# Performance work log

Hardware: AMD Instinct MI355X
Metric: run time of the kernel (lower is better)

Reference implementation:

```python
import jax, jax.numpy as jnp
import numpy as np

_EPSILON = 1e-06

def _sparsemax(z):
    # sparsemax along last axis (Martins & Astudillo 2016, sort-based projection)
    m = z.shape[-1]
    z_sorted = jnp.flip(jnp.sort(z, axis=-1), axis=-1)          # descending
    z_cum = jnp.cumsum(z_sorted, axis=-1)
    r = jnp.arange(1, m + 1, dtype=z.dtype)
    support = (1.0 + r * z_sorted) > z_cum                       # [b, m]
    k = jnp.sum(support, axis=-1, keepdims=True)                 # support size, int
    tau = (jnp.take_along_axis(z_cum, k - 1, axis=-1) - 1.0) / k.astype(z.dtype)
    return jnp.maximum(z - tau, 0.0)

def setup_inputs() -> dict:
    key = jax.random.key(0)
    ks = jax.random.split(key, 4)
    b, m, d, out = 2048, 8192, 1024, 1000
    encoder_output = jax.random.normal(ks[0], (b, d), dtype=jnp.float32)
    memory_set = jax.random.normal(ks[1], (m, d), dtype=jnp.float32)
    W1 = jax.random.normal(ks[2], (d, 2 * d), dtype=jnp.float32) * (1.0 / np.sqrt(d))
    b1 = jnp.zeros((2 * d,), dtype=jnp.float32)
    W2 = jax.random.normal(ks[3], (2 * d, out), dtype=jnp.float32) * (1.0 / np.sqrt(2 * d))
    b2 = jnp.zeros((out,), dtype=jnp.float32)
    return {"encoder_output": encoder_output, "memory_set": memory_set,
            "W1": W1, "b1": b1, "W2": W2, "b2": b2}

def reference(encoder_output, memory_set, W1, b1, W2, b2):
    # cosine distance: 1 - x_hat @ y_hat^T  (with eps inside the sqrt, as in torch code)
    x_norm = encoder_output / jnp.sqrt(jnp.sum(encoder_output * encoder_output, axis=1, keepdims=True) + _EPSILON)
    y_norm = memory_set / jnp.sqrt(jnp.sum(memory_set * memory_set, axis=1, keepdims=True) + _EPSILON)
    dist = 1.0 - jnp.matmul(x_norm, y_norm.T)                    # [b, m]
    content_weights = _sparsemax(-dist)                          # [b, m]
    memory_vector = jnp.matmul(content_weights, memory_set)      # [b, d]
    h = jax.nn.relu(jnp.matmul(memory_vector, W1) + b1)          # [b, 2d]
    output = jnp.matmul(h, W2) + b2                              # [b, out]
    return output
```

## Files before the change

kernel.cpp:

```cpp
#include <hip/hip_runtime.h>
#include <hip/hip_bf16.h>


#define TPB 256
#define CAP 1024
#define BK 64

typedef __bf16 bf16x8 __attribute__((ext_vector_type(8)));
typedef float  f32x4  __attribute__((ext_vector_type(4)));

typedef const __attribute__((address_space(1))) void* gas_ptr;
typedef __attribute__((address_space(3))) void*       las_ptr;

__device__ __forceinline__ unsigned short f2bf(float f) {
    __hip_bfloat16 h = __float2bfloat16(f);
    union { __hip_bfloat16 h; unsigned short s; } u; u.h = h; return u.s;
}
__device__ __forceinline__ float bf2f(unsigned short s) {
    union { unsigned int b; float f; } u; u.b = (unsigned int)s << 16; return u.f;
}
__device__ __forceinline__ unsigned short f2h(float f) {
    union { _Float16 h; unsigned short s; } u; u.h = (_Float16)f; return u.s;
}
__device__ __forceinline__ float h2f(unsigned short s) {
    union { unsigned short s; _Float16 h; } u; u.s = s; return (float)u.h;
}

__device__ __forceinline__ float block_reduce_sum(float v, float* sred) {
    #pragma unroll
    for (int off = 32; off > 0; off >>= 1) v += __shfl_down(v, off, 64);
    int lane = threadIdx.x & 63, wid = threadIdx.x >> 6;
    if (lane == 0) sred[wid] = v;
    __syncthreads();
    if (threadIdx.x == 0) sred[0] = sred[0] + sred[1] + sred[2] + sred[3];
    __syncthreads();
    float r = sred[0];
    __syncthreads();
    return r;
}

__device__ __forceinline__ void block_reduce_sum2(float& a, float& b, float* sred) {
    #pragma unroll
    for (int off = 32; off > 0; off >>= 1) {
        a += __shfl_down(a, off, 64);
        b += __shfl_down(b, off, 64);
    }
    int lane = threadIdx.x & 63, wid = threadIdx.x >> 6;
    if (lane == 0) { sred[wid] = a; sred[4 + wid] = b; }
    __syncthreads();
    if (threadIdx.x == 0) {
        sred[0] = sred[0] + sred[1] + sred[2] + sred[3];
        sred[4] = sred[4] + sred[5] + sred[6] + sred[7];
    }
    __syncthreads();
    a = sred[0]; b = sred[4];
    __syncthreads();
}

__global__ __launch_bounds__(TPB) void normalize_rows_bf16(const float* __restrict__ X0,
                                                           unsigned short* __restrict__ Y0,
                                                           const float* __restrict__ X1,
                                                           unsigned short* __restrict__ Y1,
                                                           float* __restrict__ norms1,
                                                           int nrow0, int cols) {
    __shared__ float sred[4];
    int r = blockIdx.x, tid = threadIdx.x;
    const float* X; unsigned short* Y; float* nn; int row;
    if (r < nrow0) { X = X0; Y = Y0; nn = nullptr; row = r; }
    else           { X = X1; Y = Y1; nn = norms1; row = r - nrow0; }
    const float4* x4 = (const float4*)(X + (size_t)row * cols);
    ushort4* y4 = (ushort4*)(Y + (size_t)row * cols);
    int n4 = cols >> 2;
    float ss = 0.f;
    for (int i = tid; i < n4; i += TPB) {
        float4 v = x4[i];
        ss += v.x * v.x + v.y * v.y + v.z * v.z + v.w * v.w;
    }
    float tot = block_reduce_sum(ss, sred);
    float nrm = sqrtf(tot + 1e-6f);
    float inv = 1.0f / nrm;
    if (nn && tid == 0) nn[row] = nrm;
    for (int i = tid; i < n4; i += TPB) {
        float4 v = x4[i];
        ushort4 o;
        o.x = f2bf(v.x * inv); o.y = f2bf(v.y * inv);
        o.z = f2bf(v.z * inv); o.w = f2bf(v.w * inv);
        y4[i] = o;
    }
}

__global__ __launch_bounds__(TPB) void transpose_cast(const float* __restrict__ in,
                                                      unsigned short* __restrict__ out,
                                                      int R, int C, int Cpad) {
    __shared__ float t[32][33];
    int x = threadIdx.x & 31, y = threadIdx.x >> 5;
    int r0 = blockIdx.y * 32, c0 = blockIdx.x * 32;
    #pragma unroll
    for (int yy = y; yy < 32; yy += 8) {
        int c = c0 + x;
        t[yy][x] = (c < C) ? in[(size_t)(r0 + yy) * C + c] : 0.f;
    }
    __syncthreads();
    #pragma unroll
    for (int yy = y; yy < 32; yy += 8) {
        int c = c0 + yy;
        if (c < Cpad)
            out[(size_t)c * R + r0 + x] = f2bf(t[x][yy]);
    }
}

__global__ __launch_bounds__(TPB) void sparsemax_compact(unsigned short* __restrict__ Zh,
                                                         const float* __restrict__ ynorm,
                                                         int* __restrict__ cnt, int m) {
    __shared__ float sz[8192];
    __shared__ float sred[8];
    __shared__ unsigned short cidx[CAP];
    __shared__ float cval[CAP];
    __shared__ unsigned int lcnt, ocnt;
    int row = blockIdx.x, tid = threadIdx.x;
    unsigned short* zrow = Zh + (size_t)row * m;
    unsigned int* prow = (unsigned int*)zrow;
    const uint4* zr8 = (const uint4*)zrow;
    int n8 = m >> 3;

    float s = 0.f, q = 0.f;
    float4* sz4 = (float4*)sz;
    for (int i = tid; i < n8; i += TPB) {
        uint4 v = zr8[i];
        float4 a, bq;
        a.x = h2f((unsigned short)(v.x & 0xffffu)); a.y = h2f((unsigned short)(v.x >> 16));
        a.z = h2f((unsigned short)(v.y & 0xffffu)); a.w = h2f((unsigned short)(v.y >> 16));
        bq.x = h2f((unsigned short)(v.z & 0xffffu)); bq.y = h2f((unsigned short)(v.z >> 16));
        bq.z = h2f((unsigned short)(v.w & 0xffffu)); bq.w = h2f((unsigned short)(v.w >> 16));
        sz4[2 * i] = a; sz4[2 * i + 1] = bq;
        s += a.x + a.y + a.z + a.w + bq.x + bq.y + bq.z + bq.w;
        q += a.x * a.x + a.y * a.y + a.z * a.z + a.w * a.w
           + bq.x * bq.x + bq.y * bq.y + bq.z * bq.z + bq.w * bq.w;
    }
    if (tid == 0) { lcnt = 0; ocnt = 0; }
    block_reduce_sum2(s, q, sred);
    float fm   = (float)m;
    float mean = s / fm;
    float sig  = sqrtf(fmaxf(q / fm - mean * mean, 0.f));
    float tau_s = (s - 1.f) / fm;
    float tau_g = mean + 2.f * sig;

    float Sg = 0.f, cg = 0.f, Ss = 0.f, cs = 0.f;
    for (int i = tid; i < m; i += TPB) {
        float z = sz[i];
        if (z > tau_g) { Sg += z - tau_g; cg += 1.f; }
        if (z > tau_s) { Ss += z - tau_s; cs += 1.f; }
    }
    block_reduce_sum2(Sg, cg, sred);
    block_reduce_sum2(Ss, cs, sred);

    float tau_lb, S_act, c_act;
    if (Sg >= 1.f) { tau_lb = tau_g; S_act = Sg + cg * tau_g; c_act = cg; }
    else           { tau_lb = tau_s; S_act = Ss + cs * tau_s; c_act = cs; }
    float tau1 = (S_act - 1.f) / c_act;
    if (tau1 < tau_lb) tau1 = tau_lb;

    for (int i = tid; i < m; i += TPB) {
        float z = sz[i];
        if (z > tau1) {
            unsigned int slot = atomicAdd(&lcnt, 1u);
            if (slot < CAP) { cidx[slot] = (unsigned short)i; cval[slot] = z; }
        }
    }
    __syncthreads();

    if (lcnt <= CAP && lcnt > 0) {
        int n = (int)lcnt;
        float tau = tau1, prev = -1.f;
        for (int it = 0; it < 64; ++it) {
            float S = 0.f, c = 0.f;
            for (int j = tid; j < n; j += TPB) {
                float z = cval[j];
                if (z > tau) { S += z; c += 1.f; }
            }
            block_reduce_sum2(S, c, sred);
            if (c < 0.5f || c == prev) break;
            tau = (S - 1.f) / c; prev = c;
        }
        for (int j = tid; j < n; j += TPB) {
            float w = cval[j] - tau;
            if (w > 0.f) {
                int idx = (int)cidx[j];
                unsigned int slot = atomicAdd(&ocnt, 1u);
                prow[slot] = ((unsigned int)idx << 16) | (unsigned int)f2bf(w * ynorm[idx]);
            }
        }
        __syncthreads();
        if (tid == 0) cnt[row] = (int)ocnt;
    } else {
        float tau = tau1, prev = -1.f;
        for (int it = 0; it < 64; ++it) {
            float S = 0.f, c = 0.f;
            for (int i = tid; i < m; i += TPB) {
                float z = sz[i];
                if (z > tau) { S += z; c += 1.f; }
            }
            block_reduce_sum2(S, c, sred);
            if (c < 0.5f || c == prev) break;
            tau = (S - 1.f) / c; prev = c;
        }
        for (int i = tid; i < m; i += TPB) {
            float w = sz[i] - tau;
            if (w > 0.f) {
                unsigned int slot = atomicAdd(&ocnt, 1u);
                prow[slot] = ((unsigned int)i << 16) | (unsigned int)f2bf(w * ynorm[i]);
            }
        }
        __syncthreads();
        if (tid == 0) cnt[row] = (int)ocnt;
    }
}

__global__ __launch_bounds__(TPB) void sparse_mv(const unsigned int* __restrict__ packed,
                                                 const int* __restrict__ cnt,
                                                 const unsigned short* __restrict__ yn,
                                                 unsigned short* __restrict__ mv,
                                                 int pitchU, int d) {
    __shared__ unsigned int sl[TPB];
    int row = blockIdx.x, tid = threadIdx.x;
    const unsigned int* prow = packed + (size_t)row * pitchU;
    int n = cnt[row];
    int c0 = tid * 4;
    float acc0 = 0.f, acc1 = 0.f, acc2 = 0.f, acc3 = 0.f;
    for (int j0 = 0; j0 < n; j0 += TPB) {
        int chunk = min(TPB, n - j0);
        __syncthreads();
        if (tid < chunk) sl[tid] = prow[j0 + tid];
        __syncthreads();
        #pragma unroll 4
        for (int jj = 0; jj < chunk; ++jj) {
            unsigned int u = sl[jj];
            int idx = (int)(u >> 16);
            float w = bf2f((unsigned short)(u & 0xffffu));
            ushort4 v = *(const ushort4*)&yn[(size_t)idx * d + c0];
            acc0 += w * bf2f(v.x);
            acc1 += w * bf2f(v.y);
            acc2 += w * bf2f(v.z);
            acc3 += w * bf2f(v.w);
        }
    }
    ushort4 o;
    o.x = f2bf(acc0); o.y = f2bf(acc1); o.z = f2bf(acc2); o.w = f2bf(acc3);
    *(ushort4*)&mv[(size_t)row * d + c0] = o;
}

template <int BN, int OUTMODE, int RELU, int HASBIAS>
__global__ __launch_bounds__(TPB) void gemm_bt(const unsigned short* __restrict__ A,
                                               const unsigned short* __restrict__ B,
                                               const float* __restrict__ bias,
                                               void* __restrict__ C,
                                               int M, int K, int lda, int NOUT, int ldc) {
    constexpr int IT = (BN == 128) ? 4 : 2;
    __shared__ unsigned short lA[128 * BK];
    __shared__ unsigned short lB[BN * BK];
    int tid = threadIdx.x;
    int lane = tid & 63, wv = tid >> 6;
    int wm = (BN == 128) ? (wv & 1) * 64 : wv * 32;
    int wn = (BN == 128) ? (wv >> 1) * 64 : 0;
    int lr = lane & 15, kq = lane >> 4;

    int rowBase = blockIdx.y * 128;
    int colBase = blockIdx.x * BN;

    f32x4 acc[IT][4] = {};

    for (int k0 = 0; k0 < K; k0 += BK) {
        #pragma unroll
        for (int l = 0; l < 4; ++l) {
            int li = l * 256 + tid;
            int row = li >> 3, s0 = li & 7;
            int seg = s0 ^ (row & 7);
            const char* g = (const char*)(A + (size_t)(rowBase + row) * lda + k0) + seg * 16;
            __builtin_amdgcn_global_load_lds((gas_ptr)g, (las_ptr)((char*)lA + li * 16), 16, 0, 0);
        }
        #pragma unroll
        for (int l = 0; l < BN / 32; ++l) {
            int li = l * 256 + tid;
            int row = li >> 3, s0 = li & 7;
            int seg = s0 ^ (row & 7);
            const char* g = (const char*)(B + (size_t)(colBase + row) * K + k0) + seg * 16;
            __builtin_amdgcn_global_load_lds((gas_ptr)g, (las_ptr)((char*)lB + li * 16), 16, 0, 0);
        }
        __syncthreads();

        #pragma unroll
        for (int h = 0; h < 2; ++h) {
            bf16x8 av[IT], bv[4];
            #pragma unroll
            for (int i = 0; i < IT; ++i) {
                int row = wm + i * 16 + lr;
                av[i] = *(const bf16x8*)((const char*)lA + row * 128
                                         + ((((h << 2) | kq) ^ (row & 7)) * 16));
            }
            #pragma unroll
            for (int j = 0; j < 4; ++j) {
                int row = wn + j * 16 + lr;
                bv[j] = *(const bf16x8*)((const char*)lB + row * 128
                                         + ((((h << 2) | kq) ^ (row & 7)) * 16));
            }
            #pragma unroll
            for (int i = 0; i < IT; ++i)
                #pragma unroll
                for (int j = 0; j < 4; ++j)
                    acc[i][j] = __builtin_amdgcn_mfma_f32_16x16x32_bf16(av[i], bv[j], acc[i][j], 0, 0, 0);
        }
        __syncthreads();
    }

    float* Cf = (float*)C;
    unsigned short* Cb = (unsigned short*)C;
    #pragma unroll
    for (int j = 0; j < 4; ++j) {
        int col = colBase + wn + j * 16 + lr;
        if (col >= NOUT) continue;
        float bv_ = HASBIAS ? bias[col] : 0.f;
        #pragma unroll
        for (int i = 0; i < IT; ++i) {
            #pragma unroll
            for (int r = 0; r < 4; ++r) {
                int row = rowBase + wm + i * 16 + kq * 4 + r;
                float v = acc[i][j][r] + bv_;
                if (RELU) v = fmaxf(v, 0.f);
                if (OUTMODE == 0)      Cf[(size_t)row * ldc + col] = v;
                else if (OUTMODE == 1) Cb[(size_t)row * ldc + col] = f2bf(v);
                else                   Cb[(size_t)row * ldc + col] = f2h(v);
            }
        }
    }
}

extern "C" void kernel_launch(void* const* d_in, const int* in_sizes, int n_in,
                              void* d_out, int out_size, void* d_ws, size_t ws_size,
                              hipStream_t stream) {
    const float* enc = (const float*)d_in[0];
    const float* mem = (const float*)d_in[1];
    const float* W1  = (const float*)d_in[2];
    const float* b1  = (const float*)d_in[3];
    const float* W2  = (const float*)d_in[4];
    const float* b2  = (const float*)d_in[5];

    const int d    = in_sizes[3] / 2;
    const int b    = in_sizes[0] / d;
    const int m    = in_sizes[1] / d;
    const int d2   = in_sizes[3];
    const int outN = in_sizes[5];
    const int outPad = 1024;

    unsigned short* xn    = (unsigned short*)d_ws;
    unsigned short* yn    = xn  + (size_t)b * d;
    float*          ynorm = (float*)(yn + (size_t)m * d);
    unsigned short* W1T   = (unsigned short*)(ynorm + m);
    unsigned short* W2T   = W1T + (size_t)d2 * d;
    unsigned short* Zh    = W2T + (size_t)outPad * d2;
    int*            cnt   = (int*)(Zh + (size_t)b * m);
    unsigned short* mv    = (unsigned short*)(cnt + b);
    unsigned short* h     = mv + (size_t)b * d;

    normalize_rows_bf16<<<b + m, TPB, 0, stream>>>(enc, xn, mem, yn, ynorm, b, d);

    transpose_cast<<<dim3(d2 / 32, d / 32), TPB, 0, stream>>>(W1, W1T, d, d2, d2);
    transpose_cast<<<dim3(outPad / 32, d2 / 32), TPB, 0, stream>>>(W2, W2T, d2, outN, outPad);

    gemm_bt<128, 2, 0, 0><<<dim3(m / 128, b / 128), TPB, 0, stream>>>(xn, yn, nullptr, Zh,
                                                                      b, d, d, m, m);
    sparsemax_compact<<<b, TPB, 0, stream>>>(Zh, ynorm, cnt, m);

    sparse_mv<<<b, TPB, 0, stream>>>((const unsigned int*)Zh, cnt, yn, mv, m / 2, d);

    gemm_bt<64, 1, 1, 1><<<dim3(d2 / 64, b / 128), TPB, 0, stream>>>(mv, W1T, b1, h,
                                                                     b, d, d, d2, d2);
    gemm_bt<64, 0, 0, 1><<<dim3(outPad / 64, b / 128), TPB, 0, stream>>>(h, W2T, b2, d_out,
                                                                         b, d2, d2, outN, outN);
}
```

Before: 275.9 us.

## Fuse sparsemax with gather, retile GEMMs, merge transposes, vectorize epilogue stores

Merges the sparsemax and sparse matrix-vector kernels into one kernel that keeps z in LDS as fp16 and accumulates the weighted memory rows directly, removing the packed intermediate write and read. GEMMs are retemplated with BM/BN parameters, BK reduced to 32, larger 256x128 tiles with 512 threads for the distance GEMM, and shuffle-packed vector stores in the epilogue. The two weight transpose launches are merged into one. The changes trade a shorter K step (more syncs per tile) and different occupancy for fewer launches and less global traffic.

```diff
diff --git a/kernel.cpp b/kernel.cpp
--- a/kernel.cpp
+++ b/kernel.cpp
@@ -4,7 +4,6 @@
 
 #define TPB 256
 #define CAP 1024
-#define BK 64
 
 typedef __bf16 bf16x8 __attribute__((ext_vector_type(8)));
 typedef float  f32x4  __attribute__((ext_vector_type(4)));
@@ -89,12 +88,11 @@
     }
 }
 
-__global__ __launch_bounds__(TPB) void transpose_cast(const float* __restrict__ in,
-                                                      unsigned short* __restrict__ out,
-                                                      int R, int C, int Cpad) {
+__device__ __forceinline__ void tc_body(const float* in, unsigned short* out,
+                                        int R, int C, int Cpad, int bx, int by) {
     __shared__ float t[32][33];
     int x = threadIdx.x & 31, y = threadIdx.x >> 5;
-    int r0 = blockIdx.y * 32, c0 = blockIdx.x * 32;
+    int r0 = by * 32, c0 = bx * 32;
     #pragma unroll
     for (int yy = y; yy < 32; yy += 8) {
         int c = c0 + x;
@@ -109,35 +107,52 @@
     }
 }
 
-__global__ __launch_bounds__(TPB) void sparsemax_compact(unsigned short* __restrict__ Zh,
-                                                         const float* __restrict__ ynorm,
-                                                         int* __restrict__ cnt, int m) {
-    __shared__ float sz[8192];
+__global__ __launch_bounds__(TPB) void transpose_cast2(const float* __restrict__ in1,
+                                                       unsigned short* __restrict__ out1,
+                                                       int R1, int C1, int Cp1,
+                                                       const float* __restrict__ in2,
+                                                       unsigned short* __restrict__ out2,
+                                                       int R2, int C2, int Cp2,
+                                                       int nblk1) {
+    int bid = blockIdx.x;
+    if (bid < nblk1) {
+        int nx = Cp1 / 32;
+        tc_body(in1, out1, R1, C1, Cp1, bid % nx, bid / nx);
+    } else {
+        bid -= nblk1;
+        int nx = Cp2 / 32;
+        tc_body(in2, out2, R2, C2, Cp2, bid % nx, bid / nx);
+    }
+}
+
+__global__ __launch_bounds__(TPB) void sparsemax_gather(const unsigned short* __restrict__ Zh,
+                                                        const float* __restrict__ ynorm,
+                                                        const unsigned short* __restrict__ yn,
+                                                        unsigned short* __restrict__ mv,
+                                                        int m, int d) {
+    __shared__ unsigned short szh[8192];
     __shared__ float sred[8];
     __shared__ unsigned short cidx[CAP];
     __shared__ float cval[CAP];
-    __shared__ unsigned int lcnt, ocnt;
+    __shared__ unsigned int lcnt;
     int row = blockIdx.x, tid = threadIdx.x;
-    unsigned short* zrow = Zh + (size_t)row * m;
-    unsigned int* prow = (unsigned int*)zrow;
-    const uint4* zr8 = (const uint4*)zrow;
+    const uint4* zr8 = (const uint4*)(Zh + (size_t)row * m);
+    uint4* sz8 = (uint4*)szh;
     int n8 = m >> 3;
 
     float s = 0.f, q = 0.f;
-    float4* sz4 = (float4*)sz;
     for (int i = tid; i < n8; i += TPB) {
         uint4 v = zr8[i];
-        float4 a, bq;
-        a.x = h2f((unsigned short)(v.x & 0xffffu)); a.y = h2f((unsigned short)(v.x >> 16));
-        a.z = h2f((unsigned short)(v.y & 0xffffu)); a.w = h2f((unsigned short)(v.y >> 16));
-        bq.x = h2f((unsigned short)(v.z & 0xffffu)); bq.y = h2f((unsigned short)(v.z >> 16));
-        bq.z = h2f((unsigned short)(v.w & 0xffffu)); bq.w = h2f((unsigned short)(v.w >> 16));
-        sz4[2 * i] = a; sz4[2 * i + 1] = bq;
-        s += a.x + a.y + a.z + a.w + bq.x + bq.y + bq.z + bq.w;
-        q += a.x * a.x + a.y * a.y + a.z * a.z + a.w * a.w
-           + bq.x * bq.x + bq.y * bq.y + bq.z * bq.z + bq.w * bq.w;
-    }
-    if (tid == 0) { lcnt = 0; ocnt = 0; }
+        sz8[i] = v;
+        unsigned int ww[4] = {v.x, v.y, v.z, v.w};
+        #pragma unroll
+        for (int k = 0; k < 4; ++k) {
+            float a = h2f((unsigned short)(ww[k] & 0xffffu));
+            float bq = h2f((unsigned short)(ww[k] >> 16));
+            s += a + bq; q += a * a + bq * bq;
+        }
+    }
+    if (tid == 0) lcnt = 0;
     block_reduce_sum2(s, q, sred);
     float fm   = (float)m;
     float mean = s / fm;
@@ -146,10 +161,18 @@
     float tau_g = mean + 2.f * sig;
 
     float Sg = 0.f, cg = 0.f, Ss = 0.f, cs = 0.f;
-    for (int i = tid; i < m; i += TPB) {
-        float z = sz[i];
-        if (z > tau_g) { Sg += z - tau_g; cg += 1.f; }
-        if (z > tau_s) { Ss += z - tau_s; cs += 1.f; }
+    for (int i = tid; i < n8; i += TPB) {
+        uint4 v = sz8[i];
+        unsigned int ww[4] = {v.x, v.y, v.z, v.w};
+        #pragma unroll
+        for (int k = 0; k < 4; ++k) {
+            float a = h2f((unsigned short)(ww[k] & 0xffffu));
+            float bq = h2f((unsigned short)(ww[k] >> 16));
+            if (a > tau_g) { Sg += a - tau_g; cg += 1.f; }
+            if (a > tau_s) { Ss += a - tau_s; cs += 1.f; }
+            if (bq > tau_g) { Sg += bq - tau_g; cg += 1.f; }
+            if (bq > tau_s) { Ss += bq - tau_s; cs += 1.f; }
+        }
     }
     block_reduce_sum2(Sg, cg, sred);
     block_reduce_sum2(Ss, cs, sred);
@@ -161,7 +184,7 @@
     if (tau1 < tau_lb) tau1 = tau_lb;
 
     for (int i = tid; i < m; i += TPB) {
-        float z = sz[i];
+        float z = h2f(szh[i]);
         if (z > tau1) {
             unsigned int slot = atomicAdd(&lcnt, 1u);
             if (slot < CAP) { cidx[slot] = (unsigned short)i; cval[slot] = z; }
@@ -169,9 +192,11 @@
     }
     __syncthreads();
 
-    if (lcnt <= CAP && lcnt > 0) {
-        int n = (int)lcnt;
-        float tau = tau1, prev = -1.f;
+    int fast = (lcnt <= CAP && lcnt > 0);
+    float tau = tau1;
+    int n = (int)lcnt;
+    if (fast) {
+        float prev = -1.f;
         for (int it = 0; it < 64; ++it) {
             float S = 0.f, c = 0.f;
             for (int j = tid; j < n; j += TPB) {
@@ -184,151 +209,166 @@
         }
         for (int j = tid; j < n; j += TPB) {
             float w = cval[j] - tau;
-            if (w > 0.f) {
-                int idx = (int)cidx[j];
-                unsigned int slot = atomicAdd(&ocnt, 1u);
-                prow[slot] = ((unsigned int)idx << 16) | (unsigned int)f2bf(w * ynorm[idx]);
-            }
+            cval[j] = (w > 0.f) ? w * ynorm[cidx[j]] : 0.f;
         }
         __syncthreads();
-        if (tid == 0) cnt[row] = (int)ocnt;
     } else {
-        float tau = tau1, prev = -1.f;
+        float prev = -1.f;
         for (int it = 0; it < 64; ++it) {
             float S = 0.f, c = 0.f;
             for (int i = tid; i < m; i += TPB) {
-                float z = sz[i];
+                float z = h2f(szh[i]);
                 if (z > tau) { S += z; c += 1.f; }
             }
             block_reduce_sum2(S, c, sred);
             if (c < 0.5f || c == prev) break;
             tau = (S - 1.f) / c; prev = c;
         }
-        for (int i = tid; i < m; i += TPB) {
-            float w = sz[i] - tau;
-            if (w > 0.f) {
-                unsigned int slot = atomicAdd(&ocnt, 1u);
-                prow[slot] = ((unsigned int)i << 16) | (unsigned int)f2bf(w * ynorm[i]);
+    }
+
+    int g = tid >> 7;
+    int c0 = (tid & 127) * 8;
+    float acc[8] = {};
+    if (fast) {
+        for (int j = g; j < n; j += 2) {
+            float w = cval[j];
+            if (w <= 0.f) continue;
+            int idx = (int)cidx[j];
+            uint4 v = *(const uint4*)&yn[(size_t)idx * d + c0];
+            unsigned int ww[4] = {v.x, v.y, v.z, v.w};
+            #pragma unroll
+            for (int k = 0; k < 4; ++k) {
+                acc[2 * k]     += w * bf2f((unsigned short)(ww[k] & 0xffffu));
+                acc[2 * k + 1] += w * bf2f((unsigned short)(ww[k] >> 16));
             }
         }
-        __syncthreads();
-        if (tid == 0) cnt[row] = (int)ocnt;
-    }
-}
-
-__global__ __launch_bounds__(TPB) void sparse_mv(const unsigned int* __restrict__ packed,
-                                                 const int* __restrict__ cnt,
-                                                 const unsigned short* __restrict__ yn,
-                                                 unsigned short* __restrict__ mv,
-                                                 int pitchU, int d) {
-    __shared__ unsigned int sl[TPB];
-    int row = blockIdx.x, tid = threadIdx.x;
-    const unsigned int* prow = packed + (size_t)row * pitchU;
-    int n = cnt[row];
-    int c0 = tid * 4;
-    float acc0 = 0.f, acc1 = 0.f, acc2 = 0.f, acc3 = 0.f;
-    for (int j0 = 0; j0 < n; j0 += TPB) {
-        int chunk = min(TPB, n - j0);
-        __syncthreads();
-        if (tid < chunk) sl[tid] = prow[j0 + tid];
-        __syncthreads();
-        #pragma unroll 4
-        for (int jj = 0; jj < chunk; ++jj) {
-            unsigned int u = sl[jj];
-            int idx = (int)(u >> 16);
-            float w = bf2f((unsigned short)(u & 0xffffu));
-            ushort4 v = *(const ushort4*)&yn[(size_t)idx * d + c0];
-            acc0 += w * bf2f(v.x);
-            acc1 += w * bf2f(v.y);
-            acc2 += w * bf2f(v.z);
-            acc3 += w * bf2f(v.w);
-        }
-    }
-    ushort4 o;
-    o.x = f2bf(acc0); o.y = f2bf(acc1); o.z = f2bf(acc2); o.w = f2bf(acc3);
-    *(ushort4*)&mv[(size_t)row * d + c0] = o;
-}
-
-template <int BN, int OUTMODE, int RELU, int HASBIAS>
-__global__ __launch_bounds__(TPB) void gemm_bt(const unsigned short* __restrict__ A,
-                                               const unsigned short* __restrict__ B,
-                                               const float* __restrict__ bias,
-                                               void* __restrict__ C,
-                                               int M, int K, int lda, int NOUT, int ldc) {
-    constexpr int IT = (BN == 128) ? 4 : 2;
-    __shared__ unsigned short lA[128 * BK];
-    __shared__ unsigned short lB[BN * BK];
+    } else {
+        for (int i = g; i < m; i += 2) {
+            float w = h2f(szh[i]) - tau;
+            if (w <= 0.f) continue;
+            w *= ynorm[i];
+            uint4 v = *(const uint4*)&yn[(size_t)i * d + c0];
+            unsigned int ww[4] = {v.x, v.y, v.z, v.w};
+            #pragma unroll
+            for (int k = 0; k < 4; ++k) {
+                acc[2 * k]     += w * bf2f((unsigned short)(ww[k] & 0xffffu));
+                acc[2 * k + 1] += w * bf2f((unsigned short)(ww[k] >> 16));
+            }
+        }
+    }
+    __syncthreads();
+    float* comb = (float*)szh;
+    if (g == 1) {
+        #pragma unroll
+        for (int k = 0; k < 8; ++k) comb[(tid & 127) * 8 + k] = acc[k];
+    }
+    __syncthreads();
+    if (g == 0) {
+        #pragma unroll
+        for (int k = 0; k < 8; ++k) acc[k] += comb[(tid & 127) * 8 + k];
+        unsigned int w0 = f2bf(acc[0]) | ((unsigned int)f2bf(acc[1]) << 16);
+        unsigned int w1 = f2bf(acc[2]) | ((unsigned int)f2bf(acc[3]) << 16);
+        unsigned int w2 = f2bf(acc[4]) | ((unsigned int)f2bf(acc[5]) << 16);
+        unsigned int w3 = f2bf(acc[6]) | ((unsigned int)f2bf(acc[7]) << 16);
+        uint4 st = {w0, w1, w2, w3};
+        *(uint4*)&mv[(size_t)row * d + c0] = st;
+    }
+}
+
+template <int BM, int BN, int OUTMODE, int RELU, int HASBIAS>
+__global__ __launch_bounds__((BM / 64) * (BN / 64) * 64)
+void gemm_bt(const unsigned short* __restrict__ A,
+             const unsigned short* __restrict__ B,
+             const float* __restrict__ bias,
+             void* __restrict__ C,
+             int M, int K, int lda, int NOUT, int ldc) {
+    constexpr int NW   = (BM / 64) * (BN / 64);
+    constexpr int TPBL = NW * 64;
+    __shared__ unsigned short lA[BM * 32];
+    __shared__ unsigned short lB[BN * 32];
     int tid = threadIdx.x;
     int lane = tid & 63, wv = tid >> 6;
-    int wm = (BN == 128) ? (wv & 1) * 64 : wv * 32;
-    int wn = (BN == 128) ? (wv >> 1) * 64 : 0;
+    int wm = (wv % (BM / 64)) * 64;
+    int wn = (wv / (BM / 64)) * 64;
     int lr = lane & 15, kq = lane >> 4;
 
-    int rowBase = blockIdx.y * 128;
+    int rowBase = blockIdx.y * BM;
     int colBase = blockIdx.x * BN;
 
-    f32x4 acc[IT][4] = {};
-
-    for (int k0 = 0; k0 < K; k0 += BK) {
-        #pragma unroll
-        for (int l = 0; l < 4; ++l) {
-            int li = l * 256 + tid;
-            int row = li >> 3, s0 = li & 7;
-            int seg = s0 ^ (row & 7);
+    f32x4 acc[4][4] = {};
+
+    for (int k0 = 0; k0 < K; k0 += 32) {
+        constexpr int AI = BM * 4 / TPBL;
+        #pragma unroll
+        for (int l = 0; l < AI; ++l) {
+            int li = l * TPBL + tid;
+            int row = li >> 2, s0 = li & 3;
+            int seg = s0 ^ ((row >> 1) & 3);
             const char* g = (const char*)(A + (size_t)(rowBase + row) * lda + k0) + seg * 16;
             __builtin_amdgcn_global_load_lds((gas_ptr)g, (las_ptr)((char*)lA + li * 16), 16, 0, 0);
         }
-        #pragma unroll
-        for (int l = 0; l < BN / 32; ++l) {
-            int li = l * 256 + tid;
-            int row = li >> 3, s0 = li & 7;
-            int seg = s0 ^ (row & 7);
+        constexpr int BI = BN * 4 / TPBL;
+        #pragma unroll
+        for (int l = 0; l < BI; ++l) {
+            int li = l * TPBL + tid;
+            int row = li >> 2, s0 = li & 3;
+            int seg = s0 ^ ((row >> 1) & 3);
             const char* g = (const char*)(B + (size_t)(colBase + row) * K + k0) + seg * 16;
             __builtin_amdgcn_global_load_lds((gas_ptr)g, (las_ptr)((char*)lB + li * 16), 16, 0, 0);
         }
         __syncthreads();
 
-        #pragma unroll
-        for (int h = 0; h < 2; ++h) {
-            bf16x8 av[IT], bv[4];
+        bf16x8 av[4], bv[4];
+        #pragma unroll
+        for (int i = 0; i < 4; ++i) {
+            int row = wm + i * 16 + lr;
+            av[i] = *(const bf16x8*)((const char*)lA + row * 64 + ((kq ^ ((row >> 1) & 3)) * 16));
+        }
+        #pragma unroll
+        for (int j = 0; j < 4; ++j) {
+            int row = wn + j * 16 + lr;
+            bv[j] = *(const bf16x8*)((const char*)lB + row * 64 + ((kq ^ ((row >> 1) & 3)) * 16));
+        }
+        #pragma unroll
+        for (int i = 0; i < 4; ++i)
             #pragma unroll
-            for (int i = 0; i < IT; ++i) {
-                int row = wm + i * 16 + lr;
-                av[i] = *(const bf16x8*)((const char*)lA + row * 128
-                                         + ((((h << 2) | kq) ^ (row & 7)) * 16));
-            }
-            #pragma unroll
-            for (int j = 0; j < 4; ++j) {
-                int row = wn + j * 16 + lr;
-                bv[j] = *(const bf16x8*)((const char*)lB + row * 128
-                                         + ((((h << 2) | kq) ^ (row & 7)) * 16));
-            }
-            #pragma unroll
-            for (int i = 0; i < IT; ++i)
-                #pragma unroll
-                for (int j = 0; j < 4; ++j)
-                    acc[i][j] = __builtin_amdgcn_mfma_f32_16x16x32_bf16(av[i], bv[j], acc[i][j], 0, 0, 0);
-        }
+            for (int j = 0; j < 4; ++j)
+                acc[i][j] = __builtin_amdgcn_mfma_f32_16x16x32_bf16(av[i], bv[j], acc[i][j], 0, 0, 0);
         __syncthreads();
     }
 
     float* Cf = (float*)C;
     unsigned short* Cb = (unsigned short*)C;
+    bool fullN = (colBase + BN) <= NOUT;
     #pragma unroll
     for (int j = 0; j < 4; ++j) {
         int col = colBase + wn + j * 16 + lr;
-        if (col >= NOUT) continue;
-        float bv_ = HASBIAS ? bias[col] : 0.f;
-        #pragma unroll
-        for (int i = 0; i < IT; ++i) {
+        float bv_ = (HASBIAS && col < NOUT) ? bias[col] : 0.f;
+        #pragma unroll
+        for (int i = 0; i < 4; ++i) {
             #pragma unroll
             for (int r = 0; r < 4; ++r) {
                 int row = rowBase + wm + i * 16 + kq * 4 + r;
                 float v = acc[i][j][r] + bv_;
                 if (RELU) v = fmaxf(v, 0.f);
-                if (OUTMODE == 0)      Cf[(size_t)row * ldc + col] = v;
-                else if (OUTMODE == 1) Cb[(size_t)row * ldc + col] = f2bf(v);
-                else                   Cb[(size_t)row * ldc + col] = f2h(v);
+                if (OUTMODE == 0) {
+                    float p = __shfl_xor(v, 1, 64);
+                    if (fullN) {
+                        if (!(lr & 1)) { float2 st = {v, p}; *(float2*)&Cf[(size_t)row * ldc + col] = st; }
+                    } else if (col < NOUT) {
+                        Cf[(size_t)row * ldc + col] = v;
+                    }
+                } else {
+                    unsigned int hh = (OUTMODE == 1) ? (unsigned int)f2bf(v) : (unsigned int)f2h(v);
+                    unsigned int p1 = (unsigned int)__shfl_xor((int)hh, 1, 64);
+                    unsigned int u = (hh & 0xffffu) | (p1 << 16);
+                    unsigned int p2 = (unsigned int)__shfl_xor((int)u, 2, 64);
+                    if (fullN) {
+                        if (!(lr & 3)) { uint2 st = {u, p2}; *(uint2*)&Cb[(size_t)row * ldc + col] = st; }
+                    } else if (col < NOUT) {
+                        Cb[(size_t)row * ldc + col] = (unsigned short)hh;
+                    }
+                }
             }
         }
     }
@@ -357,23 +397,24 @@
     unsigned short* W1T   = (unsigned short*)(ynorm + m);
     unsigned short* W2T   = W1T + (size_t)d2 * d;
     unsigned short* Zh    = W2T + (size_t)outPad * d2;
-    int*            cnt   = (int*)(Zh + (size_t)b * m);
-    unsigned short* mv    = (unsigned short*)(cnt + b);
+    unsigned short* mv    = Zh + (size_t)b * m;
     unsigned short* h     = mv + (size_t)b * d;
 
     normalize_rows_bf16<<<b + m, TPB, 0, stream>>>(enc, xn, mem, yn, ynorm, b, d);
 
-    transpose_cast<<<dim3(d2 / 32, d / 32), TPB, 0, stream>>>(W1, W1T, d, d2, d2);
-    transpose_cast<<<dim3(outPad / 32, d2 / 32), TPB, 0, stream>>>(W2, W2T, d2, outN, outPad);
-
-    gemm_bt<128, 2, 0, 0><<<dim3(m / 128, b / 128), TPB, 0, stream>>>(xn, yn, nullptr, Zh,
-                                                                      b, d, d, m, m);
-    sparsemax_compact<<<b, TPB, 0, stream>>>(Zh, ynorm, cnt, m);
-
-    sparse_mv<<<b, TPB, 0, stream>>>((const unsigned int*)Zh, cnt, yn, mv, m / 2, d);
-
-    gemm_bt<64, 1, 1, 1><<<dim3(d2 / 64, b / 128), TPB, 0, stream>>>(mv, W1T, b1, h,
-                                                                     b, d, d, d2, d2);
-    gemm_bt<64, 0, 0, 1><<<dim3(outPad / 64, b / 128), TPB, 0, stream>>>(h, W2T, b2, d_out,
-                                                                         b, d2, d2, outN, outN);
-}
+    int nblk1 = (d2 / 32) * (d / 32);
+    int nblk2 = (outPad / 32) * (d2 / 32);
+    transpose_cast2<<<nblk1 + nblk2, TPB, 0, stream>>>(W1, W1T, d, d2, d2,
+                                                       W2, W2T, d2, outN, outPad, nblk1);
+
+    gemm_bt<256, 128, 2, 0, 0><<<dim3(m / 128, b / 256), 512, 0, stream>>>(
+        xn, yn, nullptr, Zh, b, d, d, m, m);
+
+    sparsemax_gather<<<b, TPB, 0, stream>>>(Zh, ynorm, yn, mv, m, d);
+
+    gemm_bt<128, 128, 1, 1, 1><<<dim3(d2 / 128, b / 128), 256, 0, stream>>>(
+        mv, W1T, b1, h, b, d, d, d2, d2);
+
+    gemm_bt<128, 64, 0, 0, 1><<<dim3(outPad / 64, b / 128), 128, 0, stream>>>(
+        h, W2T, b2, d_out, b, d2, d2, outN, outN);
+}
```

Measured after the change: 301.9 us. +9.4%, slower.
